# Performance work log

Hardware: AMD Instinct MI355X
Metric: run time of the kernel (lower is better)

The kernel has to match this reference:

```python
import jax, jax.numpy as jnp
import numpy as np

B, S, D, H = 2, 2048, 1024, 16
HD = D // H
EPS = 1e-5


def layer_norm(x, g, b):
    m = jnp.mean(x, axis=-1, keepdims=True)
    v = jnp.mean(jnp.square(x - m), axis=-1, keepdims=True)
    return (x - m) * jax.lax.rsqrt(v + EPS) * g + b


def setup_inputs() -> dict:
    key = jax.random.key(0)
    ks = jax.random.split(key, 16)
    s = 0.02
    x = jax.random.normal(ks[0], (B, S, D), dtype=jnp.float32)
    mask = jax.random.randint(ks[1], (1, 1, S, S), 0, 2, dtype=jnp.int32)
    return {
        "x": x,
        "mask": mask,
        "Wq": jax.random.normal(ks[2], (D, D), jnp.float32) * s,
        "Wk": jax.random.normal(ks[3], (D, D), jnp.float32) * s,
        "Wv": jax.random.normal(ks[4], (D, D), jnp.float32) * s,
        "Wo": jax.random.normal(ks[5], (D, D), jnp.float32) * s,
        "bo": jax.random.normal(ks[6], (D,), jnp.float32) * s,
        "ln1_g": jnp.ones((D,), jnp.float32),
        "ln1_b": jnp.zeros((D,), jnp.float32),
        "W1": jax.random.normal(ks[7], (D, 4 * D), jnp.float32) * s,
        "b1": jax.random.normal(ks[8], (4 * D,), jnp.float32) * s,
        "W2": jax.random.normal(ks[9], (4 * D, D), jnp.float32) * s,
        "b2": jax.random.normal(ks[10], (D,), jnp.float32) * s,
        "ln2_g": jnp.ones((D,), jnp.float32),
        "ln2_b": jnp.zeros((D,), jnp.float32),
    }


def reference(x, mask, Wq, Wk, Wv, Wo, bo, ln1_g, ln1_b, W1, b1, W2, b2, ln2_g, ln2_b):
    # --- multi-head attention (dropout = identity in eval) ---
    q = (x @ Wq).reshape(B, S, H, HD)
    k = (x @ Wk).reshape(B, S, H, HD)
    v = (x @ Wv).reshape(B, S, H, HD)
    scores = jnp.einsum("bshd,bthd->bhst", q, k) / jnp.sqrt(jnp.float32(HD))
    scores = jnp.where(mask == 1, jnp.float32(-1e9), scores)
    p = jax.nn.softmax(scores, axis=-1)
    o = jnp.einsum("bhst,bthd->bshd", p, v).reshape(B, S, D)
    attn_out = o @ Wo + bo
    # --- residual with norm on the branch (note: norm applied to attn output) ---
    x = x + layer_norm(attn_out, ln1_g, ln1_b)
    # --- FFN: gelu after fc1 AND after fc2 (as in source) ---
    h = jax.nn.gelu(x @ W1 + b1, approximate=False)
    h = jax.nn.gelu(h @ W2 + b2, approximate=False)
    x = x + layer_norm(h, ln2_g, ln2_b)
    return x
```

## Files before the change

### kernel.cpp

```cpp
#include <hip/hip_runtime.h>
#include <hip/hip_bf16.h>
#include <cstdint>

#define BB 2
#define SS 2048
#define DD 1024
#define HH 16
#define HDIM 64
#define MROWS (BB*SS)

typedef __bf16 bf16;
using bf16x8 = __bf16 __attribute__((ext_vector_type(8)));
using bf16x4 = __bf16 __attribute__((ext_vector_type(4)));
using bf16x2 = __bf16 __attribute__((ext_vector_type(2)));
using f32x4  = float __attribute__((ext_vector_type(4)));

__device__ __forceinline__ float gelu_exact(float x) {
    return 0.5f * x * (1.f + erff(x * 0.70710678118654752f));
}

__device__ __forceinline__ void stage16(const bf16* g, bf16* lds_chunk_base, int lane) {
#if __has_builtin(__builtin_amdgcn_global_load_lds)
    __builtin_amdgcn_global_load_lds((const __attribute__((address_space(1))) void*)g,
                                     (__attribute__((address_space(3))) void*)lds_chunk_base,
                                     16, 0, 0);
#else
    *(bf16x8*)(lds_chunk_base + lane * 8) = *(const bf16x8*)g;
#endif
}

__device__ __forceinline__ unsigned lds_addr(const void* p) {
    return (unsigned)(uintptr_t)(const __attribute__((address_space(3))) void*)p;
}

__device__ __forceinline__ bf16x8 dsr(unsigned addr) {
    bf16x8 r;
    asm volatile("ds_read_b128 %0, %1" : "=v"(r) : "v"(addr));
    return r;
}

__global__ __launch_bounds__(256) void prep_kernel(
    const float* __restrict__ x, bf16* __restrict__ x_b,
    const int* __restrict__ mask, unsigned long long* __restrict__ maskb,
    const float* __restrict__ Wq, const float* __restrict__ Wk,
    const float* __restrict__ Wv, const float* __restrict__ Wo,
    const float* __restrict__ W1, const float* __restrict__ W2,
    bf16* __restrict__ Wqkv_t, bf16* __restrict__ Wo_t,
    bf16* __restrict__ W1_t, bf16* __restrict__ W2_t) {
    const int bid = blockIdx.x;
    if (bid < 4096) {
        int i = bid * 256 + threadIdx.x;
        float4 v = ((const float4*)x)[i];
        bf16x4 o;
        o[0] = (bf16)v.x; o[1] = (bf16)v.y; o[2] = (bf16)v.z; o[3] = (bf16)v.w;
        *(bf16x4*)(x_b + (size_t)i * 4) = o;
        return;
    }
    if (bid < 20480) {
        int gid = (bid - 4096) * 256 + threadIdx.x;
        int mv = mask[gid];
        unsigned long long bal = __ballot(mv == 1);
        if ((threadIdx.x & 63) == 0) maskb[gid >> 6] = bal;
        return;
    }
    int t = bid - 20480;
    const float* W; bf16* Wt; int K, N, bxn, byk;
    if (t < 1024) {
        int wsel = t >> 8;
        int tt = t & 255;
        W  = (wsel == 0) ? Wq : (wsel == 1) ? Wk : (wsel == 2) ? Wv : Wo;
        Wt = (wsel == 3) ? Wo_t : (Wqkv_t + (size_t)wsel * 1024 * 1024);
        K = 1024; N = 1024; bxn = (tt & 15) * 64; byk = (tt >> 4) * 64;
    } else if (t < 2048) {
        int tt = t - 1024;
        W = W1; Wt = W1_t; K = 1024; N = 4096;
        bxn = (tt & 63) * 64; byk = (tt >> 6) * 64;
    } else {
        int tt = t - 2048;
        W = W2; Wt = W2_t; K = 4096; N = 1024;
        bxn = (tt & 15) * 64; byk = (tt >> 4) * 64;
    }
    __shared__ float tile[64][65];
    const int tx = threadIdx.x & 15;
    const int ty = threadIdx.x >> 4;
#pragma unroll
    for (int j = 0; j < 4; ++j) {
        float4 v = *(const float4*)(W + (size_t)(byk + ty + 16 * j) * N + bxn + tx * 4);
        tile[ty + 16 * j][tx * 4 + 0] = v.x;
        tile[ty + 16 * j][tx * 4 + 1] = v.y;
        tile[ty + 16 * j][tx * 4 + 2] = v.z;
        tile[ty + 16 * j][tx * 4 + 3] = v.w;
    }
    __syncthreads();
    const int r  = threadIdx.x >> 2;
    const int c0 = (threadIdx.x & 3) * 16;
#pragma unroll
    for (int j = 0; j < 4; ++j) {
        bf16x4 ov;
#pragma unroll
        for (int i = 0; i < 4; ++i) ov[i] = (bf16)tile[c0 + 4 * j + i][r];
        *(bf16x4*)(Wt + (size_t)(bxn + r) * K + byk + c0 + 4 * j) = ov;
    }
}

template <int EPI>
__global__ __launch_bounds__(256, 3) void gemm_bt(const bf16* __restrict__ A,
                                                  const bf16* __restrict__ Bt,
                                                  void* __restrict__ C,
                                                  void* __restrict__ C2,
                                                  const float* __restrict__ bias,
                                                  int M, int N, int K, int ldk) {
    __shared__ __align__(16) bf16 As[128 * 64];
    __shared__ __align__(16) bf16 Bs[128 * 64];
    const int tid  = threadIdx.x;
    const int lane = tid & 63;
    const int wave = tid >> 6;
    const int l16  = lane & 15;
    const int quad = lane >> 4;
    const int wm = wave >> 1, wn = wave & 1;

    int bx, by, bz;
    {
        const int Gx = gridDim.x, Gy = gridDim.y, Gz = gridDim.z;
        const int nwg = Gx * Gy * Gz;
        int L = blockIdx.x + Gx * (blockIdx.y + Gy * blockIdx.z);
        if ((nwg & 7) == 0) {
            int chunk = nwg >> 3;
            L = (L & 7) * chunk + (L >> 3);
        }
        bx = L % Gx; int rest = L / Gx; by = rest % Gy; bz = rest / Gy;
    }
    const int m0 = by * 128, n0 = bx * 128;
    const int z  = bz;
    A  += (size_t)z * K;
    Bt += (size_t)z * K;

    f32x4 acc[4][4];
#pragma unroll
    for (int i = 0; i < 4; ++i)
#pragma unroll
        for (int j = 0; j < 4; ++j) acc[i][j] = (f32x4){0.f, 0.f, 0.f, 0.f};

    const int nsteps = K >> 6;
    for (int kt = 0; kt < nsteps; ++kt) {
        const int kbase = kt << 6;
#pragma unroll
        for (int c = 0; c < 4; ++c) {
            int chunk = wave * 4 + c;
            int gi = chunk * 64 + lane;
            int m  = gi >> 3;
            int cp = gi & 7;
            int g  = cp ^ (m & 7);
            stage16(A  + (size_t)(m0 + m) * ldk + kbase + g * 8, As + chunk * 512, lane);
            stage16(Bt + (size_t)(n0 + m) * ldk + kbase + g * 8, Bs + chunk * 512, lane);
        }
        __syncthreads();
#pragma unroll
        for (int ks = 0; ks < 2; ++ks) {
            bf16x8 af[4], bfr[4];
#pragma unroll
            for (int i = 0; i < 4; ++i) {
                int m = wm * 64 + i * 16 + l16;
                int g = ks * 4 + quad;
                af[i]  = *(const bf16x8*)(As + m * 64 + ((g ^ (m & 7)) * 8));
                int n = wn * 64 + i * 16 + l16;
                bfr[i] = *(const bf16x8*)(Bs + n * 64 + ((g ^ (n & 7)) * 8));
            }
#pragma unroll
            for (int i = 0; i < 4; ++i)
#pragma unroll
                for (int j = 0; j < 4; ++j)
                    acc[i][j] = __builtin_amdgcn_mfma_f32_16x16x32_bf16(af[i], bfr[j], acc[i][j], 0, 0, 0);
        }
        __syncthreads();
    }

    float* Cz = (EPI == 4) ? (z ? (float*)C2 : (float*)C) : nullptr;
#pragma unroll
    for (int i = 0; i < 4; ++i) {
        int row = m0 + wm * 64 + i * 16 + quad * 4;
#pragma unroll
        for (int j = 0; j < 4; ++j) {
            int col = n0 + wn * 64 + j * 16 + l16;
            float bv = (EPI == 2) ? bias[col] : 0.f;
#pragma unroll
            for (int r = 0; r < 4; ++r) {
                float v = acc[i][j][r];
                if (EPI == 2) v = gelu_exact(v + bv);
                size_t idx = (size_t)(row + r) * N + col;
                if (EPI == 4) Cz[idx] = v;
                else          ((bf16*)C)[idx] = (bf16)v;
            }
        }
    }
}

template <int EPI>
__global__ __launch_bounds__(512, 2) void gemm256(const bf16* __restrict__ A,
                                                  const bf16* __restrict__ Bt,
                                                  void* __restrict__ C0, void* __restrict__ C1,
                                                  void* __restrict__ C2v, void* __restrict__ C3,
                                                  const float* __restrict__ bias,
                                                  int M, int N, int K, int ldk) {
    __shared__ __align__(16) bf16 As[2 * 16384];
    __shared__ __align__(16) bf16 Bs[2 * 16384];
    const int tid  = threadIdx.x;
    const int lane = tid & 63;
    const int wave = tid >> 6;
    const int l16  = lane & 15;
    const int quad = lane >> 4;
    const int wm = wave >> 2;
    const int wn = wave & 3;

    int bx, by, bz;
    {
        const int Gx = gridDim.x, Gy = gridDim.y, Gz = gridDim.z;
        const int nwg = Gx * Gy * Gz;
        int L = blockIdx.x + Gx * (blockIdx.y + Gy * blockIdx.z);
        if ((nwg & 7) == 0) {
            int chunk = nwg >> 3;
            L = (L & 7) * chunk + (L >> 3);
        }
        bx = L % Gx; int rest = L / Gx; by = rest % Gy; bz = rest / Gy;
    }
    const int m0 = by * 256, n0 = bx * 256;
    const int z  = bz;
    A  += (size_t)z * K;
    Bt += (size_t)z * K;

    const int grow = wave * 8 + (lane >> 3);
    const int gg   = (lane & 7) ^ (grow & 7);
    const bf16* sA = A  + (size_t)(m0 + grow) * ldk + gg * 8;
    const bf16* sB = Bt + (size_t)(n0 + grow) * ldk + gg * 8;
    const int dchunk = wave * 512;

    const unsigned s7 = (unsigned)(l16 & 7);
    const unsigned e0 = ((unsigned)quad ^ s7) * 16;
    const unsigned arow0 = (unsigned)(wm * 128 + l16) * 128;
    const unsigned brow0 = (unsigned)(wn * 64 + l16) * 128;
    const unsigned asBase = lds_addr(As);
    const unsigned bsBase = lds_addr(Bs);

    f32x4 acc[8][4];
#pragma unroll
    for (int i = 0; i < 8; ++i)
#pragma unroll
        for (int j = 0; j < 4; ++j) acc[i][j] = (f32x4){0.f, 0.f, 0.f, 0.f};

    const int nt = K >> 6;

    auto stageHalf = [&](int t, int R0, bool isB) {
        const int kb = t << 6;
        const bf16* s = isB ? sB : sA;
        bf16* d = (isB ? Bs : As) + (t & 1) * 16384 + R0 * 64 + dchunk;
        stage16(s + (size_t)R0 * ldk + kb, d, lane);
        stage16(s + (size_t)(R0 + 64) * ldk + kb, d + 4096, lane);
    };

    stageHalf(0, 0, false); stageHalf(0, 128, false);
    stageHalf(0, 0, true);  stageHalf(0, 128, true);
    if (1 < nt) {
        stageHalf(1, 0, false);
        asm volatile("s_waitcnt vmcnt(2)");
    } else {
        asm volatile("s_waitcnt vmcnt(0)");
    }
    __builtin_amdgcn_s_barrier();

    for (int t = 0; t < nt; ++t) {
        const unsigned ab = asBase + (unsigned)(t & 1) * 32768 + arow0;
        const unsigned bb = bsBase + (unsigned)(t & 1) * 32768 + brow0;
        bf16x8 af[4][2], b0[2][2], b1[2][2];

#pragma unroll
        for (int i = 0; i < 4; ++i) {
            af[i][0] = dsr(ab + i * 2048 + e0);
            af[i][1] = dsr(ab + i * 2048 + (e0 ^ 64));
        }
#pragma unroll
        for (int j = 0; j < 2; ++j) {
            b0[j][0] = dsr(bb + j * 2048 + e0);
            b0[j][1] = dsr(bb + j * 2048 + (e0 ^ 64));
        }
        if (t + 1 < nt) { stageHalf(t + 1, 128, false); stageHalf(t + 1, 0, true); }
        __builtin_amdgcn_s_barrier();
        asm volatile("s_waitcnt lgkmcnt(0)");
        __builtin_amdgcn_sched_barrier(0);
        __builtin_amdgcn_s_setprio(1);
#pragma unroll
        for (int i = 0; i < 4; ++i)
#pragma unroll
            for (int j = 0; j < 2; ++j)
#pragma unroll
                for (int kk = 0; kk < 2; ++kk)
                    acc[i][j] = __builtin_amdgcn_mfma_f32_16x16x32_bf16(af[i][kk], b0[j][kk], acc[i][j], 0, 0, 0);
        __builtin_amdgcn_s_setprio(0);
        __builtin_amdgcn_s_barrier();

#pragma unroll
        for (int j = 0; j < 2; ++j) {
            b1[j][0] = dsr(bb + 4096 + j * 2048 + e0);
            b1[j][1] = dsr(bb + 4096 + j * 2048 + (e0 ^ 64));
        }
        if (t + 1 < nt) stageHalf(t + 1, 128, true);
        __builtin_amdgcn_s_barrier();
        asm volatile("s_waitcnt lgkmcnt(0)");
        __builtin_amdgcn_sched_barrier(0);
        __builtin_amdgcn_s_setprio(1);
#pragma unroll
        for (int i = 0; i < 4; ++i)
#pragma unroll
            for (int j = 0; j < 2; ++j)
#pragma unroll
                for (int kk = 0; kk < 2; ++kk)
                    acc[i][j + 2] = __builtin_amdgcn_mfma_f32_16x16x32_bf16(af[i][kk], b1[j][kk], acc[i][j + 2], 0, 0, 0);
        __builtin_amdgcn_s_setprio(0);
        __builtin_amdgcn_s_barrier();

#pragma unroll
        for (int i = 0; i < 4; ++i) {
            af[i][0] = dsr(ab + 8192 + i * 2048 + e0);
            af[i][1] = dsr(ab + 8192 + i * 2048 + (e0 ^ 64));
        }
        __builtin_amdgcn_s_barrier();
        asm volatile("s_waitcnt lgkmcnt(0)");
        __builtin_amdgcn_sched_barrier(0);
        __builtin_amdgcn_s_setprio(1);
#pragma unroll
        for (int i = 0; i < 4; ++i)
#pragma unroll
            for (int j = 0; j < 2; ++j)
#pragma unroll
                for (int kk = 0; kk < 2; ++kk)
                    acc[i + 4][j + 2] = __builtin_amdgcn_mfma_f32_16x16x32_bf16(af[i][kk], b1[j][kk], acc[i + 4][j + 2], 0, 0, 0);
        __builtin_amdgcn_s_setprio(0);
        __builtin_amdgcn_s_barrier();

        if (t + 2 < nt) stageHalf(t + 2, 0, false);
        __builtin_amdgcn_s_barrier();
        __builtin_amdgcn_s_setprio(1);
#pragma unroll
        for (int i = 0; i < 4; ++i)
#pragma unroll
            for (int j = 0; j < 2; ++j)
#pragma unroll
                for (int kk = 0; kk < 2; ++kk)
                    acc[i + 4][j] = __builtin_amdgcn_mfma_f32_16x16x32_bf16(af[i][kk], b0[j][kk], acc[i + 4][j], 0, 0, 0);
        __builtin_amdgcn_s_setprio(0);
        if (t + 2 < nt) { asm volatile("s_waitcnt vmcnt(2)"); }
        else            { asm volatile("s_waitcnt vmcnt(0)"); }
        __builtin_amdgcn_s_barrier();
    }

    float* Cz = nullptr;
    if (EPI == 4) Cz = (z == 0) ? (float*)C0 : (z == 1) ? (float*)C1 : (z == 2) ? (float*)C2v : (float*)C3;
#pragma unroll
    for (int i = 0; i < 8; ++i) {
        int row = m0 + wm * 128 + i * 16 + quad * 4;
#pragma unroll
        for (int j = 0; j < 4; ++j) {
            int col = n0 + wn * 64 + j * 16 + l16;
            float bv = (EPI == 2) ? bias[col] : 0.f;
#pragma unroll
            for (int r = 0; r < 4; ++r) {
                float v = acc[i][j][r];
                if (EPI == 2) v = gelu_exact(v + bv);
                size_t idx = (size_t)(row + r) * N + col;
                if (EPI == 4) Cz[idx] = v;
                else          ((bf16*)C0)[idx] = (bf16)v;
            }
        }
    }
}

__global__ __launch_bounds__(512, 2) void flash_attn(const bf16* __restrict__ qkv,
                                                     const unsigned long long* __restrict__ maskb,
                                                     bf16* __restrict__ o) {
    __shared__ __align__(16) bf16 Ks[2 * 128 * 64];
    __shared__ __align__(16) bf16 Vts[2 * 64 * 136];
    const int tid  = threadIdx.x;
    const int lane = tid & 63;
    const int wave = tid >> 6;
    const int l16  = lane & 15;
    const int quad = lane >> 4;

    int bqx, bhy;
    {
        const int Gx = gridDim.x, Gy = gridDim.y;
        int L = blockIdx.x + Gx * blockIdx.y;
        int chunk = (Gx * Gy) >> 3;
        L = (L & 7) * chunk + (L >> 3);
        bqx = L % Gx; bhy = L / Gx;
    }
    const int bh = bhy;
    const int b = bh >> 4, h = bh & 15;
    const int q0 = bqx * 128;
    const size_t rowb = (size_t)b * SS;
    const float SCL = 0.18033688011112042f;

    const size_t qrow = (rowb + q0 + wave * 16 + l16) * 3072 + h * 64;
    bf16x8 qf[2];
    {
        bf16x8 q0r = *(const bf16x8*)(qkv + qrow + quad * 8);
        bf16x8 q1r = *(const bf16x8*)(qkv + qrow + 32 + quad * 8);
#pragma unroll
        for (int j = 0; j < 8; ++j) {
            qf[0][j] = (bf16)((float)q0r[j] * SCL);
            qf[1][j] = (bf16)((float)q1r[j] * SCL);
        }
    }

    f32x4 oacc[4];
#pragma unroll
    for (int d = 0; d < 4; ++d) oacc[d] = (f32x4){0.f, 0.f, 0.f, 0.f};
    f32x4 lacc = (f32x4){0.f, 0.f, 0.f, 0.f};
    const int mrow32 = (q0 + wave * 16 + l16) * 32;

    bf16x8 ones;
#pragma unroll
    for (int j = 0; j < 8; ++j) ones[j] = (bf16)1.0f;

    const int vt_tc = (lane >> 4) * 32 + ((lane >> 1) & 3) * 8 + ((lane >> 3) & 1) * 4 + 2 * (lane & 1);
    const int vd8 = wave * 8;

    int kst[2], ksg[2];
#pragma unroll
    for (int c = 0; c < 2; ++c) {
        int gi = (wave * 2 + c) * 64 + lane;
        kst[c] = gi >> 3;
        ksg[c] = (gi & 7) ^ (kst[c] & 7);
    }

    bf16x8 kreg[2], vreg[2];
    ulonglong2 mwreg;
    auto loadKV = [&](int t0) {
#pragma unroll
        for (int c = 0; c < 2; ++c)
            kreg[c] = *(const bf16x8*)(qkv + (rowb + t0 + kst[c]) * 3072 + 1024 + h * 64 + ksg[c] * 8);
        const bf16* vg = qkv + (rowb + t0 + 2 * lane) * 3072 + 2048 + h * 64 + vd8;
        vreg[0] = *(const bf16x8*)(vg);
        vreg[1] = *(const bf16x8*)(vg + 3072);
    };
    auto commitKV = [&](int buf) {
        bf16* Ksq = Ks + buf * 8192;
        bf16* Vtsq = Vts + buf * 8704;
#pragma unroll
        for (int c = 0; c < 2; ++c)
            *(bf16x8*)(Ksq + (wave * 2 + c) * 512 + lane * 8) = kreg[c];
#pragma unroll
        for (int j = 0; j < 8; ++j) {
            bf16x2 pr; pr[0] = vreg[0][j]; pr[1] = vreg[1][j];
            *(bf16x2*)(Vtsq + (vd8 + j) * 136 + vt_tc) = pr;
        }
    };

    loadKV(0);
    mwreg = *(const ulonglong2*)(maskb + mrow32);
    commitKV(0);
    loadKV(128);
    __syncthreads();

    const int NT = SS / 128;
    for (int kt = 0; kt < NT; ++kt) {
        ulonglong2 mw = mwreg;
        if (kt + 1 < NT) {
            commitKV((kt + 1) & 1);
            mwreg = *(const ulonglong2*)(maskb + mrow32 + (kt + 1) * 2);
            if (kt + 2 < NT) loadKV((kt + 2) * 128);
        }

        const bf16* Ksp = Ks + (kt & 1) * 8192;
        const bf16* Vtsp = Vts + (kt & 1) * 8704;

        f32x4 st[8];
        __builtin_amdgcn_s_setprio(1);
#pragma unroll
        for (int tg = 0; tg < 8; ++tg) {
            int tl = tg * 16 + l16;
            bf16x8 a0 = *(const bf16x8*)(Ksp + tl * 64 + ((quad       ^ (tl & 7)) * 8));
            bf16x8 a1 = *(const bf16x8*)(Ksp + tl * 64 + (((4 + quad) ^ (tl & 7)) * 8));
            f32x4 s = (f32x4){0.f, 0.f, 0.f, 0.f};
            s = __builtin_amdgcn_mfma_f32_16x16x32_bf16(a0, qf[0], s, 0, 0, 0);
            s = __builtin_amdgcn_mfma_f32_16x16x32_bf16(a1, qf[1], s, 0, 0, 0);
            st[tg] = s;
        }
        __builtin_amdgcn_s_setprio(0);

        unsigned long long s0 = mw.x >> (quad * 4);
        unsigned long long s1 = mw.y >> (quad * 4);
        bf16x8 pva[4];
#pragma unroll
        for (int tg = 0; tg < 8; ++tg) {
            unsigned int bits = (unsigned int)(((tg < 4) ? s0 : s1) >> ((tg & 3) * 16));
#pragma unroll
            for (int r = 0; r < 4; ++r) {
                float p = __builtin_amdgcn_exp2f(st[tg][r]);
                p = ((bits >> r) & 1u) ? 0.f : p;
                pva[tg >> 1][(tg & 1) * 4 + r] = (bf16)p;
            }
        }

        __builtin_amdgcn_s_setprio(1);
#pragma unroll
        for (int kc = 0; kc < 4; ++kc) {
#pragma unroll
            for (int dg = 0; dg < 4; ++dg) {
                bf16x8 bfrag = *(const bf16x8*)(Vtsp + (dg * 16 + l16) * 136 + kc * 32 + quad * 8);
                oacc[dg] = __builtin_amdgcn_mfma_f32_16x16x32_bf16(pva[kc], bfrag, oacc[dg], 0, 0, 0);
            }
            lacc = __builtin_amdgcn_mfma_f32_16x16x32_bf16(pva[kc], ones, lacc, 0, 0, 0);
        }
        __builtin_amdgcn_s_setprio(0);

        __syncthreads();
    }

#pragma unroll
    for (int r = 0; r < 4; ++r) {
        float inv_l = 1.f / lacc[r];
        bf16* orow = o + (rowb + q0 + wave * 16 + quad * 4 + r) * DD + h * 64;
#pragma unroll
        for (int dg = 0; dg < 4; ++dg)
            orow[dg * 16 + l16] = (bf16)(oacc[dg][r] * inv_l);
    }
}

template <bool GELU, bool WB16, int NP>
__global__ __launch_bounds__(256) void ln_fused(const float* __restrict__ resid,
                                                const float* __restrict__ p0,
                                                const float* __restrict__ p1,
                                                const float* __restrict__ p2,
                                                const float* __restrict__ p3,
                                                const float* __restrict__ bias,
                                                const float* __restrict__ g,
                                                const float* __restrict__ bb,
                                                float* __restrict__ outf,
                                                bf16* __restrict__ outb) {
    const int row = blockIdx.x;
    const int tid = threadIdx.x;
    const size_t base = (size_t)row * DD + tid * 4;
    float4 a0 = *(const float4*)(p0 + base);
    float4 a1 = *(const float4*)(p1 + base);
    float4 bz = *(const float4*)(bias + tid * 4);
    float ax = a0.x + a1.x + bz.x;
    float ay = a0.y + a1.y + bz.y;
    float az = a0.z + a1.z + bz.z;
    float aw = a0.w + a1.w + bz.w;
    if (NP == 4) {
        float4 a2 = *(const float4*)(p2 + base);
        float4 a3 = *(const float4*)(p3 + base);
        ax += a2.x + a3.x; ay += a2.y + a3.y; az += a2.z + a3.z; aw += a2.w + a3.w;
    }
    if (GELU) { ax = gelu_exact(ax); ay = gelu_exact(ay); az = gelu_exact(az); aw = gelu_exact(aw); }
    float s1 = ax + ay + az + aw;
    float s2 = ax * ax + ay * ay + az * az + aw * aw;
#pragma unroll
    for (int off = 32; off; off >>= 1) {
        s1 += __shfl_xor(s1, off, 64);
        s2 += __shfl_xor(s2, off, 64);
    }
    __shared__ float red[8];
    if ((tid & 63) == 0) { red[(tid >> 6) * 2] = s1; red[(tid >> 6) * 2 + 1] = s2; }
    __syncthreads();
    s1 = red[0] + red[2] + red[4] + red[6];
    s2 = red[1] + red[3] + red[5] + red[7];
    float mean = s1 * (1.f / DD);
    float var  = s2 * (1.f / DD) - mean * mean;
    float rs = rsqrtf(var + 1e-5f);
    float4 gv = *(const float4*)(g + tid * 4);
    float4 bv = *(const float4*)(bb + tid * 4);
    float4 rv = *(const float4*)(resid + base);
    float y0 = rv.x + (ax - mean) * rs * gv.x + bv.x;
    float y1 = rv.y + (ay - mean) * rs * gv.y + bv.y;
    float y2 = rv.z + (az - mean) * rs * gv.z + bv.z;
    float y3 = rv.w + (aw - mean) * rs * gv.w + bv.w;
    float4 yo = make_float4(y0, y1, y2, y3);
    *(float4*)(outf + base) = yo;
    if (WB16) {
        bf16x4 ob;
        ob[0] = (bf16)y0; ob[1] = (bf16)y1; ob[2] = (bf16)y2; ob[3] = (bf16)y3;
        *(bf16x4*)(outb + base) = ob;
    }
}

extern "C" void kernel_launch(void* const* d_in, const int* in_sizes, int n_in,
                              void* d_out, int out_size, void* d_ws, size_t ws_size,
                              hipStream_t stream) {
    const float* x    = (const float*)d_in[0];
    const int*   mask = (const int*)d_in[1];
    const float* Wq   = (const float*)d_in[2];
    const float* Wk   = (const float*)d_in[3];
    const float* Wv   = (const float*)d_in[4];
    const float* Wo   = (const float*)d_in[5];
    const float* bo   = (const float*)d_in[6];
    const float* ln1g = (const float*)d_in[7];
    const float* ln1b = (const float*)d_in[8];
    const float* W1   = (const float*)d_in[9];
    const float* b1   = (const float*)d_in[10];
    const float* W2   = (const float*)d_in[11];
    const float* b2   = (const float*)d_in[12];
    const float* ln2g = (const float*)d_in[13];
    const float* ln2b = (const float*)d_in[14];

    char* w = (char*)d_ws;
    bf16* Wqkv_t = (bf16*)w; w += (size_t)3072 * 1024 * 2;
    bf16* Wo_t   = (bf16*)w; w += (size_t)1024 * 1024 * 2;
    bf16* W1_t   = (bf16*)w; w += (size_t)4096 * 1024 * 2;
    bf16* W2_t   = (bf16*)w; w += (size_t)1024 * 4096 * 2;
    bf16* x_b    = (bf16*)w; w += (size_t)MROWS * DD * 2;
    bf16* qkv    = (bf16*)w; w += (size_t)MROWS * 3072 * 2;
    float* R     = (float*)w; w += (size_t)MROWS * DD * 8;
    float* x1_f  = (float*)w; w += (size_t)MROWS * DD * 4;
    unsigned long long* maskb = (unsigned long long*)w; w += (size_t)SS * 32 * 8;
    bf16* o_b  = x_b;
    bf16* x1_b = x_b;
    float* op0 = R;
    float* op1 = R + (size_t)MROWS * DD;
    bf16*  h_b = (bf16*)R;
    float* fp0 = (float*)d_out;
    float* fp1 = (float*)x_b;
    float* fp2 = (float*)x_b + (size_t)4 * 1024 * 1024;
    float* fp3 = (float*)d_ws;

    prep_kernel<<<23552, 256, 0, stream>>>(x, x_b, mask, maskb,
                                           Wq, Wk, Wv, Wo, W1, W2,
                                           Wqkv_t, Wo_t, W1_t, W2_t);

    gemm256<0><<<dim3(12, 16, 1), 512, 0, stream>>>(x_b, Wqkv_t, qkv, nullptr, nullptr, nullptr, nullptr, MROWS, 3072, 1024, 1024);
    flash_attn<<<dim3(SS / 128, BB * HH), 512, 0, stream>>>(qkv, maskb, o_b);
    gemm_bt<4><<<dim3(8, 32, 2), 256, 0, stream>>>(o_b, Wo_t, op0, op1, nullptr, MROWS, 1024, 512, 1024);
    ln_fused<false, true, 2><<<MROWS, 256, 0, stream>>>(x, op0, op1, nullptr, nullptr, bo, ln1g, ln1b, x1_f, x1_b);
    gemm256<2><<<dim3(16, 16, 1), 512, 0, stream>>>(x1_b, W1_t, h_b, nullptr, nullptr, nullptr, b1, MROWS, 4096, 1024, 1024);
    gemm256<4><<<dim3(4, 16, 4), 512, 0, stream>>>(h_b, W2_t, fp0, fp1, fp2, fp3, nullptr, MROWS, 1024, 1024, 4096);
    ln_fused<true, false, 4><<<MROWS, 256, 0, stream>>>(x1_f, fp0, fp1, fp2, fp3, b2, ln2g, ln2b, (float*)d_out, nullptr);
}
```

Baseline: 370.6 us.

## Unroll GEMM main loop by two and remap wave tiles to half-block quadrants

```diff
diff --git a/kernel.cpp b/kernel.cpp
--- a/kernel.cpp
+++ b/kernel.cpp
@@ -236,8 +236,9 @@
 
     const unsigned s7 = (unsigned)(l16 & 7);
     const unsigned e0 = ((unsigned)quad ^ s7) * 16;
-    const unsigned arow0 = (unsigned)(wm * 128 + l16) * 128;
-    const unsigned brow0 = (unsigned)(wn * 64 + l16) * 128;
+    const unsigned arow_lo = (unsigned)(wm * 64 + l16) * 128;
+    const unsigned brow_lo = (unsigned)(wn * 32 + l16) * 128;
+    const unsigned HIOFF = 16384u;
     const unsigned asBase = lds_addr(As);
     const unsigned bsBase = lds_addr(Bs);
 
@@ -257,32 +258,29 @@
         stage16(s + (size_t)(R0 + 64) * ldk + kb, d + 4096, lane);
     };
 
-    stageHalf(0, 0, false); stageHalf(0, 128, false);
-    stageHalf(0, 0, true);  stageHalf(0, 128, true);
-    if (1 < nt) {
-        stageHalf(1, 0, false);
-        asm volatile("s_waitcnt vmcnt(2)");
-    } else {
-        asm volatile("s_waitcnt vmcnt(0)");
-    }
+    stageHalf(0, 0, false); stageHalf(0, 0, true);
+    stageHalf(0, 128, true); stageHalf(0, 128, false);
+    stageHalf(1, 0, false); stageHalf(1, 128, true); stageHalf(1, 128, false);
+    asm volatile("s_waitcnt vmcnt(6)");
     __builtin_amdgcn_s_barrier();
 
-    for (int t = 0; t < nt; ++t) {
-        const unsigned ab = asBase + (unsigned)(t & 1) * 32768 + arow0;
-        const unsigned bb = bsBase + (unsigned)(t & 1) * 32768 + brow0;
-        bf16x8 af[4][2], b0[2][2], b1[2][2];
+    for (int T = 0; T < nt; T += 2) {
+        const bool more = (T + 2 < nt);
+        const unsigned a0b = asBase,           b0b = bsBase;
+        const unsigned a1b = asBase + 32768u,  b1b = bsBase + 32768u;
+        bf16x8 af[4][2], bl[2][2], bh[2][2];
 
 #pragma unroll
         for (int i = 0; i < 4; ++i) {
-            af[i][0] = dsr(ab + i * 2048 + e0);
-            af[i][1] = dsr(ab + i * 2048 + (e0 ^ 64));
+            af[i][0] = dsr(a0b + arow_lo + i * 2048 + e0);
+            af[i][1] = dsr(a0b + arow_lo + i * 2048 + (e0 ^ 64));
         }
 #pragma unroll
         for (int j = 0; j < 2; ++j) {
-            b0[j][0] = dsr(bb + j * 2048 + e0);
-            b0[j][1] = dsr(bb + j * 2048 + (e0 ^ 64));
-        }
-        if (t + 1 < nt) { stageHalf(t + 1, 128, false); stageHalf(t + 1, 0, true); }
+            bl[j][0] = dsr(b0b + brow_lo + j * 2048 + e0);
+            bl[j][1] = dsr(b0b + brow_lo + j * 2048 + (e0 ^ 64));
+        }
+        stageHalf(T + 1, 0, true);
         __builtin_amdgcn_s_barrier();
         asm volatile("s_waitcnt lgkmcnt(0)");
         __builtin_amdgcn_sched_barrier(0);
@@ -293,16 +291,16 @@
             for (int j = 0; j < 2; ++j)
 #pragma unroll
                 for (int kk = 0; kk < 2; ++kk)
-                    acc[i][j] = __builtin_amdgcn_mfma_f32_16x16x32_bf16(af[i][kk], b0[j][kk], acc[i][j], 0, 0, 0);
+                    acc[i][j] = __builtin_amdgcn_mfma_f32_16x16x32_bf16(af[i][kk], bl[j][kk], acc[i][j], 0, 0, 0);
         __builtin_amdgcn_s_setprio(0);
         __builtin_amdgcn_s_barrier();
 
 #pragma unroll
         for (int j = 0; j < 2; ++j) {
-            b1[j][0] = dsr(bb + 4096 + j * 2048 + e0);
-            b1[j][1] = dsr(bb + 4096 + j * 2048 + (e0 ^ 64));
-        }
-        if (t + 1 < nt) stageHalf(t + 1, 128, true);
+            bh[j][0] = dsr(b0b + brow_lo + HIOFF + j * 2048 + e0);
+            bh[j][1] = dsr(b0b + brow_lo + HIOFF + j * 2048 + (e0 ^ 64));
+        }
+        if (more) stageHalf(T + 2, 0, false);
         __builtin_amdgcn_s_barrier();
         asm volatile("s_waitcnt lgkmcnt(0)");
         __builtin_amdgcn_sched_barrier(0);
@@ -313,15 +311,16 @@
             for (int j = 0; j < 2; ++j)
 #pragma unroll
                 for (int kk = 0; kk < 2; ++kk)
-                    acc[i][j + 2] = __builtin_amdgcn_mfma_f32_16x16x32_bf16(af[i][kk], b1[j][kk], acc[i][j + 2], 0, 0, 0);
+                    acc[i][j + 2] = __builtin_amdgcn_mfma_f32_16x16x32_bf16(af[i][kk], bh[j][kk], acc[i][j + 2], 0, 0, 0);
         __builtin_amdgcn_s_setprio(0);
         __builtin_amdgcn_s_barrier();
 
 #pragma unroll
         for (int i = 0; i < 4; ++i) {
-            af[i][0] = dsr(ab + 8192 + i * 2048 + e0);
-            af[i][1] = dsr(ab + 8192 + i * 2048 + (e0 ^ 64));
-        }
+            af[i][0] = dsr(a0b + arow_lo + HIOFF + i * 2048 + e0);
+            af[i][1] = dsr(a0b + arow_lo + HIOFF + i * 2048 + (e0 ^ 64));
+        }
+        if (more) stageHalf(T + 2, 128, true);
         __builtin_amdgcn_s_barrier();
         asm volatile("s_waitcnt lgkmcnt(0)");
         __builtin_amdgcn_sched_barrier(0);
@@ -332,11 +331,11 @@
             for (int j = 0; j < 2; ++j)
 #pragma unroll
                 for (int kk = 0; kk < 2; ++kk)
-                    acc[i + 4][j + 2] = __builtin_amdgcn_mfma_f32_16x16x32_bf16(af[i][kk], b1[j][kk], acc[i + 4][j + 2], 0, 0, 0);
-        __builtin_amdgcn_s_setprio(0);
-        __builtin_amdgcn_s_barrier();
-
-        if (t + 2 < nt) stageHalf(t + 2, 0, false);
+                    acc[i + 4][j + 2] = __builtin_amdgcn_mfma_f32_16x16x32_bf16(af[i][kk], bh[j][kk], acc[i + 4][j + 2], 0, 0, 0);
+        __builtin_amdgcn_s_setprio(0);
+        __builtin_amdgcn_s_barrier();
+
+        if (more) stageHalf(T + 2, 128, false);
         __builtin_amdgcn_s_barrier();
         __builtin_amdgcn_s_setprio(1);
 #pragma unroll
@@ -345,10 +344,90 @@
             for (int j = 0; j < 2; ++j)
 #pragma unroll
                 for (int kk = 0; kk < 2; ++kk)
-                    acc[i + 4][j] = __builtin_amdgcn_mfma_f32_16x16x32_bf16(af[i][kk], b0[j][kk], acc[i + 4][j], 0, 0, 0);
-        __builtin_amdgcn_s_setprio(0);
-        if (t + 2 < nt) { asm volatile("s_waitcnt vmcnt(2)"); }
-        else            { asm volatile("s_waitcnt vmcnt(0)"); }
+                    acc[i + 4][j] = __builtin_amdgcn_mfma_f32_16x16x32_bf16(af[i][kk], bl[j][kk], acc[i + 4][j], 0, 0, 0);
+        __builtin_amdgcn_s_setprio(0);
+        if (more) { asm volatile("s_waitcnt vmcnt(6)"); }
+        else      { asm volatile("s_waitcnt vmcnt(0)"); }
+        __builtin_amdgcn_s_barrier();
+
+#pragma unroll
+        for (int i = 0; i < 4; ++i) {
+            af[i][0] = dsr(a1b + arow_lo + i * 2048 + e0);
+            af[i][1] = dsr(a1b + arow_lo + i * 2048 + (e0 ^ 64));
+        }
+#pragma unroll
+        for (int j = 0; j < 2; ++j) {
+            bl[j][0] = dsr(b1b + brow_lo + j * 2048 + e0);
+            bl[j][1] = dsr(b1b + brow_lo + j * 2048 + (e0 ^ 64));
+        }
+        if (more) stageHalf(T + 2, 0, true);
+        __builtin_amdgcn_s_barrier();
+        asm volatile("s_waitcnt lgkmcnt(0)");
+        __builtin_amdgcn_sched_barrier(0);
+        __builtin_amdgcn_s_setprio(1);
+#pragma unroll
+        for (int i = 0; i < 4; ++i)
+#pragma unroll
+            for (int j = 0; j < 2; ++j)
+#pragma unroll
+                for (int kk = 0; kk < 2; ++kk)
+                    acc[i][j] = __builtin_amdgcn_mfma_f32_16x16x32_bf16(af[i][kk], bl[j][kk], acc[i][j], 0, 0, 0);
+        __builtin_amdgcn_s_setprio(0);
+        __builtin_amdgcn_s_barrier();
+
+#pragma unroll
+        for (int j = 0; j < 2; ++j) {
+            bh[j][0] = dsr(b1b + brow_lo + HIOFF + j * 2048 + e0);
+            bh[j][1] = dsr(b1b + brow_lo + HIOFF + j * 2048 + (e0 ^ 64));
+        }
+        if (more) stageHalf(T + 3, 0, false);
+        __builtin_amdgcn_s_barrier();
+        asm volatile("s_waitcnt lgkmcnt(0)");
+        __builtin_amdgcn_sched_barrier(0);
+        __builtin_amdgcn_s_setprio(1);
+#pragma unroll
+        for (int i = 0; i < 4; ++i)
+#pragma unroll
+            for (int j = 0; j < 2; ++j)
+#pragma unroll
+                for (int kk = 0; kk < 2; ++kk)
+                    acc[i][j + 2] = __builtin_amdgcn_mfma_f32_16x16x32_bf16(af[i][kk], bh[j][kk], acc[i][j + 2], 0, 0, 0);
+        __builtin_amdgcn_s_setprio(0);
+        __builtin_amdgcn_s_barrier();
+
+#pragma unroll
+        for (int i = 0; i < 4; ++i) {
+            af[i][0] = dsr(a1b + arow_lo + HIOFF + i * 2048 + e0);
+            af[i][1] = dsr(a1b + arow_lo + HIOFF + i * 2048 + (e0 ^ 64));
+        }
+        if (more) stageHalf(T + 3, 128, true);
+        __builtin_amdgcn_s_barrier();
+        asm volatile("s_waitcnt lgkmcnt(0)");
+        __builtin_amdgcn_sched_barrier(0);
+        __builtin_amdgcn_s_setprio(1);
+#pragma unroll
+        for (int i = 0; i < 4; ++i)
+#pragma unroll
+            for (int j = 0; j < 2; ++j)
+#pragma unroll
+                for (int kk = 0; kk < 2; ++kk)
+                    acc[i + 4][j + 2] = __builtin_amdgcn_mfma_f32_16x16x32_bf16(af[i][kk], bh[j][kk], acc[i + 4][j + 2], 0, 0, 0);
+        __builtin_amdgcn_s_setprio(0);
+        __builtin_amdgcn_s_barrier();
+
+        if (more) stageHalf(T + 3, 128, false);
+        __builtin_amdgcn_s_barrier();
+        __builtin_amdgcn_s_setprio(1);
+#pragma unroll
+        for (int i = 0; i < 4; ++i)
+#pragma unroll
+            for (int j = 0; j < 2; ++j)
+#pragma unroll
+                for (int kk = 0; kk < 2; ++kk)
+                    acc[i + 4][j] = __builtin_amdgcn_mfma_f32_16x16x32_bf16(af[i][kk], bl[j][kk], acc[i + 4][j], 0, 0, 0);
+        __builtin_amdgcn_s_setprio(0);
+        if (more) { asm volatile("s_waitcnt vmcnt(6)"); }
+        else      { asm volatile("s_waitcnt vmcnt(0)"); }
         __builtin_amdgcn_s_barrier();
     }
 
@@ -356,10 +435,12 @@
     if (EPI == 4) Cz = (z == 0) ? (float*)C0 : (z == 1) ? (float*)C1 : (z == 2) ? (float*)C2v : (float*)C3;
 #pragma unroll
     for (int i = 0; i < 8; ++i) {
-        int row = m0 + wm * 128 + i * 16 + quad * 4;
+        int rbase = (i < 4) ? (wm * 64 + i * 16) : (128 + wm * 64 + (i - 4) * 16);
+        int row = m0 + rbase + quad * 4;
 #pragma unroll
         for (int j = 0; j < 4; ++j) {
-            int col = n0 + wn * 64 + j * 16 + l16;
+            int cbase = (j < 2) ? (wn * 32 + j * 16) : (128 + wn * 32 + (j - 2) * 16);
+            int col = n0 + cbase + l16;
             float bv = (EPI == 2) ? bias[col] : 0.f;
 #pragma unroll
             for (int r = 0; r < 4; ++r) {
```

Measured after the change: 429.5 us. +15.9%, slower.
